# Optimization experiments

Measured on AMD Instinct MI355X. Metric: run time of the kernel, lower is better.

Reference implementation:

```python
import jax, jax.numpy as jnp
import numpy as np
from jax import lax

DIM = 64
HEADS = 4
GN_EPS = 1e-5
L2_EPS = 1e-12


def conv2d(x, w, b=None, pad=0, groups=1, dil=1):
    out = lax.conv_general_dilated(
        x, w, window_strides=(1, 1), padding=[(pad, pad), (pad, pad)],
        rhs_dilation=(dil, dil), dimension_numbers=('NCHW', 'OIHW', 'NCHW'),
        feature_group_count=groups)
    if b is not None:
        out = out + b[None, :, None, None]
    return out


def group_norm2(x, gamma, beta):
    # GroupNorm with 2 groups over (C/2, H, W)
    b, c, h, w = x.shape
    xr = x.reshape(b, 2, c // 2, h, w)
    mu = xr.mean(axis=(2, 3, 4), keepdims=True)
    var = xr.var(axis=(2, 3, 4), keepdims=True)
    xn = ((xr - mu) * lax.rsqrt(var + GN_EPS)).reshape(b, c, h, w)
    return xn * gamma[None, :, None, None] + beta[None, :, None, None]


def lka(x, c0w, c0b, csw, csb, c1w, c1b, gn_g, gn_b):
    dim = c0w.shape[0]
    a = conv2d(x, c0w, c0b, pad=2, groups=dim)           # depthwise 5x5
    a = conv2d(a, csw, csb, pad=3, groups=dim, dil=3)    # depthwise 3x3, dilation 3
    a = conv2d(a, c1w, c1b, pad=0)                       # 1x1 pointwise
    return jax.nn.leaky_relu(group_norm2(a, gn_g, gn_b), 0.2)


def l2norm_lastdim(t):
    n = jnp.sqrt(jnp.sum(t * t, axis=-1, keepdims=True))
    return t / jnp.maximum(n, L2_EPS)


def setup_inputs() -> dict:
    key = jax.random.key(0)
    ks = jax.random.split(key, 24)
    B, C, H, W = 4, DIM, 256, 256
    s = 0.05

    def rn(k, shape, scale=s):
        return jax.random.normal(k, shape, dtype=jnp.float32) * scale

    d2 = 2 * DIM
    inp = {
        'x': jax.random.normal(ks[0], (B, C, H, W), dtype=jnp.float32),
        'y': jax.random.normal(ks[1], (B, C, H, W), dtype=jnp.float32),
        # 1x1 projections (bias=False)
        'kv_w': rn(ks[2], (d2, DIM, 1, 1)),
        'q_w': rn(ks[3], (DIM, DIM, 1, 1)),
        'proj_w': rn(ks[4], (DIM, DIM, 1, 1)),
        # kv LKA (C_hid = C_out = 128)
        'kv_c0_w': rn(ks[5], (d2, 1, 5, 5)), 'kv_c0_b': rn(ks[6], (d2,)),
        'kv_cs_w': rn(ks[7], (d2, 1, 3, 3)), 'kv_cs_b': rn(ks[8], (d2,)),
        'kv_c1_w': rn(ks[9], (d2, d2, 1, 1)), 'kv_c1_b': rn(ks[10], (d2,)),
        'kv_gn_g': jnp.ones((d2,), jnp.float32), 'kv_gn_b': jnp.zeros((d2,), jnp.float32),
        # q LKA (C_hid = C_out = 64)
        'q_c0_w': rn(ks[11], (DIM, 1, 5, 5)), 'q_c0_b': rn(ks[12], (DIM,)),
        'q_cs_w': rn(ks[13], (DIM, 1, 3, 3)), 'q_cs_b': rn(ks[14], (DIM,)),
        'q_c1_w': rn(ks[15], (DIM, DIM, 1, 1)), 'q_c1_b': rn(ks[16], (DIM,)),
        'q_gn_g': jnp.ones((DIM,), jnp.float32), 'q_gn_b': jnp.zeros((DIM,), jnp.float32),
        'temperature': jnp.ones((HEADS, 1, 1), jnp.float32),
    }
    return inp


def reference(x, y, kv_w, q_w, proj_w,
              kv_c0_w, kv_c0_b, kv_cs_w, kv_cs_b, kv_c1_w, kv_c1_b, kv_gn_g, kv_gn_b,
              q_c0_w, q_c0_b, q_cs_w, q_cs_b, q_c1_w, q_c1_b, q_gn_g, q_gn_b,
              temperature):
    b, c, h, w = x.shape
    kv = lka(conv2d(y, kv_w), kv_c0_w, kv_c0_b, kv_cs_w, kv_cs_b, kv_c1_w, kv_c1_b, kv_gn_g, kv_gn_b)
    k, v = jnp.split(kv, 2, axis=1)
    q = lka(conv2d(x, q_w), q_c0_w, q_c0_b, q_cs_w, q_cs_b, q_c1_w, q_c1_b, q_gn_g, q_gn_b)

    ch = c // HEADS
    hw = h * w
    q = q.reshape(b, HEADS, ch, hw)
    k = k.reshape(b, HEADS, ch, hw)
    v = v.reshape(b, HEADS, ch, hw)

    q = l2norm_lastdim(q)
    k = l2norm_lastdim(k)

    attn = jnp.einsum('bhcn,bhdn->bhcd', q, k) * temperature[None]  # [b,H,ch,ch]
    attn = jax.nn.softmax(attn, axis=-1)
    out = jnp.einsum('bhcd,bhdn->bhcn', attn, v).reshape(b, c, h, w)
    return conv2d(out, proj_w)
```

## Files before the change

kernel.cpp:

```cpp
#include <hip/hip_runtime.h>

#define HW 65536
#define IMG 256

__device__ __forceinline__ float hsum4(float4 v) { return v.x + v.y + v.z + v.w; }
__device__ __forceinline__ float lrelu(float v) { return v >= 0.f ? v : 0.2f * v; }

template<int CIT, int NW, bool GNIN, bool DUAL>
__global__ __launch_bounds__(NW*64)
void conv1x1_v5(const float* __restrict__ in, int in_cs,
                const float* __restrict__ in2, int in2_cs,
                const float* __restrict__ w, int w_bstride,
                const float* __restrict__ bias,
                float* __restrict__ out, int out_cs, int out_coff,
                float* __restrict__ stats, int gsel,
                const float* __restrict__ gstats,
                const float* __restrict__ g_gamma, const float* __restrict__ g_beta,
                int g_coff, float g_Nf)
{
    const int b  = blockIdx.y;
    const int j  = threadIdx.x & 63;
    const int wv = __builtin_amdgcn_readfirstlane((int)(threadIdx.x >> 6));
    const int co0 = wv * 16;
    const int q0 = blockIdx.x * 64;
    const float* wb = w + (size_t)b * w_bstride;

    float gmean = 0.f, grstd = 0.f;
    if (GNIN) {
        gmean = gstats[b*4] / g_Nf;
        float var = gstats[b*4 + 1] / g_Nf - gmean * gmean;
        grstd = rsqrtf(var + 1e-5f);
    }

    float4 acc[16];
    #pragma unroll
    for (int k = 0; k < 16; ++k) {
        float bv = bias ? bias[co0 + k] : 0.f;
        acc[k] = make_float4(bv, bv, bv, bv);
    }

    const float4* in4a = (const float4*)in + (size_t)b * in_cs * (HW/4) + q0 + j;

    auto run = [&](const float4* base, const float* wrb, int n) {
        #pragma unroll 4
        for (int ci = 0; ci < n; ++ci) {
            float4 x = base[(size_t)ci * (HW/4)];
            if (GNIN) {
                float A = g_gamma[g_coff + ci] * grstd;
                float B = g_beta[g_coff + ci] - gmean * A;
                x.x = lrelu(fmaf(x.x, A, B));
                x.y = lrelu(fmaf(x.y, A, B));
                x.z = lrelu(fmaf(x.z, A, B));
                x.w = lrelu(fmaf(x.w, A, B));
            }
            const float* wr = wrb + ci;
            #pragma unroll
            for (int k = 0; k < 16; ++k) {
                float wk = wr[(size_t)(co0 + k) * CIT];
                acc[k].x = fmaf(wk, x.x, acc[k].x);
                acc[k].y = fmaf(wk, x.y, acc[k].y);
                acc[k].z = fmaf(wk, x.z, acc[k].z);
                acc[k].w = fmaf(wk, x.w, acc[k].w);
            }
        }
    };

    if (DUAL) {
        const float4* in4b = (const float4*)in2 + (size_t)b * in2_cs * (HW/4) + q0 + j;
        run(in4a, wb, 64);
        run(in4b, wb + 64, 64);
    } else {
        run(in4a, wb, CIT);
    }

    if (!GNIN && stats) {
        float s = 0.f, ss = 0.f;
        #pragma unroll
        for (int k = 0; k < 16; ++k) {
            s  += acc[k].x + acc[k].y + acc[k].z + acc[k].w;
            ss += acc[k].x*acc[k].x + acc[k].y*acc[k].y
                + acc[k].z*acc[k].z + acc[k].w*acc[k].w;
        }
        #pragma unroll
        for (int o = 32; o; o >>= 1) { s += __shfl_down(s, o, 64); ss += __shfl_down(ss, o, 64); }
        if (j == 0) {
            int g = 0;
            if (gsel == -1) g = (co0 >= 32) ? 1 : 0;
            else if (gsel == -2) g = (co0 >= 64) ? 1 : 0;
            float* st = stats + (size_t)b*4 + g*2;
            atomicAdd(st,     s);
            atomicAdd(st + 1, ss);
        }
    }

    float4* out4 = (float4*)out + ((size_t)b * out_cs + out_coff) * (HW/4) + q0 + j;
    #pragma unroll
    for (int k = 0; k < 16; ++k)
        out4[(size_t)(co0 + k) * (HW/4)] = acc[k];
}

__global__ __launch_bounds__(256)
void dwfused(const float* __restrict__ in, int in_cs, int in_coff,
             const float* __restrict__ w5, const float* __restrict__ b5, int w5_coff,
             const float* __restrict__ w3, const float* __restrict__ b3, int w3_coff,
             float* __restrict__ out, int out_cs, int out_coff)
{
    constexpr int TH = 32, TW = 64;
    constexpr int IN_H = TH + 10, IN_W = TW + 10;
    constexpr int MID_H = TH + 6, MID_W = TW + 6;
    constexpr int IN_RS = IN_W + 2;
    constexpr int MID_RS = MID_W + 2;
    __shared__ float Xs[IN_H * IN_RS];
    __shared__ float Ms[MID_H * MID_RS];
    const int z = blockIdx.z;
    const int c = z & 63, b = z >> 6;
    const int x0 = blockIdx.x * TW, y0 = blockIdx.y * TH;
    const float* ip = in + ((size_t)b*in_cs + in_coff + c) * HW;

    float wk5[25];
    #pragma unroll
    for (int i = 0; i < 25; ++i) wk5[i] = w5[(size_t)(w5_coff + c)*25 + i];
    const float bv5 = b5[w5_coff + c];
    float wk3[9];
    #pragma unroll
    for (int i = 0; i < 9; ++i) wk3[i] = w3[(size_t)(w3_coff + c)*9 + i];
    const float bv3 = b3[w3_coff + c];

    for (int idx = threadIdx.x; idx < IN_H*IN_W; idx += 256) {
        int ly = idx / IN_W, lx = idx - ly*IN_W;
        int gy = y0 + ly - 5, gx = x0 + lx - 5;
        float v = 0.f;
        if (gy >= 0 && gy < IMG && gx >= 0 && gx < IMG)
            v = ip[gy*IMG + gx];
        Xs[ly*IN_RS + lx] = v;
    }
    __syncthreads();

    for (int idx = threadIdx.x; idx < MID_H*MID_W; idx += 256) {
        int my = idx / MID_W, mx = idx - my*MID_W;
        int gy = y0 + my - 3, gx = x0 + mx - 3;
        float v = 0.f;
        if (gy >= 0 && gy < IMG && gx >= 0 && gx < IMG) {
            v = bv5;
            #pragma unroll
            for (int ky = 0; ky < 5; ++ky) {
                const float* xr = &Xs[(my + ky)*IN_RS + mx];
                #pragma unroll
                for (int kx = 0; kx < 5; ++kx)
                    v = fmaf(wk5[ky*5 + kx], xr[kx], v);
            }
        }
        Ms[my*MID_RS + mx] = v;
    }
    __syncthreads();

    const int qx = (threadIdx.x & 15) * 4;
    const int ly0 = threadIdx.x >> 4;
    float* op = out + ((size_t)b*out_cs + out_coff + c) * HW;
    #pragma unroll
    for (int r = 0; r < 2; ++r) {
        const int oy = ly0 + r*16;
        float o0 = bv3, o1 = bv3, o2 = bv3, o3 = bv3;
        #pragma unroll
        for (int kt = 0; kt < 3; ++kt) {
            const float* mr = &Ms[(oy + 3*kt)*MID_RS + qx];
            #pragma unroll
            for (int kx = 0; kx < 3; ++kx) {
                float wv_ = wk3[kt*3 + kx];
                o0 = fmaf(wv_, mr[3*kx + 0], o0);
                o1 = fmaf(wv_, mr[3*kx + 1], o1);
                o2 = fmaf(wv_, mr[3*kx + 2], o2);
                o3 = fmaf(wv_, mr[3*kx + 3], o3);
            }
        }
        *(float4*)(op + (size_t)(y0 + oy)*IMG + x0 + qx) = make_float4(o0, o1, o2, o3);
    }
}

__global__ __launch_bounds__(256)
void attn_dot_v4(const float* __restrict__ q, const float* __restrict__ k, int k_cs,
                 const float* __restrict__ stQ, const float* __restrict__ stK,
                 const float* __restrict__ qg, const float* __restrict__ qb,
                 const float* __restrict__ kg, const float* __restrict__ kb,
                 float* __restrict__ attn_raw,
                 float* __restrict__ ssq, float* __restrict__ ssk)
{
    __shared__ float4 qs[2048], ks[2048];
    __shared__ float sred[512];
    const int h = blockIdx.y, b = blockIdx.z;
    const int t0 = blockIdx.x * 128;
    const int cc = threadIdx.x & 15;
    const int ch = h*16 + cc;

    const int gq = (ch >= 32) ? 1 : 0;
    float mq = stQ[b*4 + gq*2] / (32.f * HW);
    float vq = stQ[b*4 + gq*2 + 1] / (32.f * HW) - mq*mq;
    const float Aq = qg[ch] * rsqrtf(vq + 1e-5f);
    const float Bq = qb[ch] - mq * Aq;
    float mk = stK[b*4] / (64.f * HW);
    float vk = stK[b*4 + 1] / (64.f * HW) - mk*mk;
    const float Ak = kg[ch] * rsqrtf(vk + 1e-5f);
    const float Bk = kb[ch] - mk * Ak;

    const float4* q4 = (const float4*)q + ((size_t)b*64   + ch) * (HW/4) + t0;
    const float4* k4 = (const float4*)k + ((size_t)b*k_cs + ch) * (HW/4) + t0;
    float sq_acc = 0.f, sk_acc = 0.f;
    #pragma unroll
    for (int s = 0; s < 8; ++s) {
        int t = (threadIdx.x >> 4) + s*16;
        float4 v = q4[t];
        v.x = lrelu(fmaf(v.x, Aq, Bq)); v.y = lrelu(fmaf(v.y, Aq, Bq));
        v.z = lrelu(fmaf(v.z, Aq, Bq)); v.w = lrelu(fmaf(v.w, Aq, Bq));
        sq_acc += v.x*v.x + v.y*v.y + v.z*v.z + v.w*v.w;
        qs[t*16 + cc] = v;
        float4 u = k4[t];
        u.x = lrelu(fmaf(u.x, Ak, Bk)); u.y = lrelu(fmaf(u.y, Ak, Bk));
        u.z = lrelu(fmaf(u.z, Ak, Bk)); u.w = lrelu(fmaf(u.w, Ak, Bk));
        sk_acc += u.x*u.x + u.y*u.y + u.z*u.z + u.w*u.w;
        ks[t*16 + cc] = u;
    }
    sred[threadIdx.x]       = sq_acc;
    sred[256 + threadIdx.x] = sk_acc;
    __syncthreads();

    const int p   = threadIdx.x & 63;
    const int sub = threadIdx.x >> 6;
    const int c0 = (p >> 3) << 1, d0 = (p & 7) << 1;
    float4 a00 = make_float4(0,0,0,0), a01 = a00, a10 = a00, a11 = a00;
    #pragma unroll
    for (int i = 0; i < 32; ++i) {
        int t = sub*32 + i;
        float4 qa = qs[t*16 + c0], qb_ = qs[t*16 + c0 + 1];
        float4 ka = ks[t*16 + d0], kb_ = ks[t*16 + d0 + 1];
        a00.x = fmaf(qa.x, ka.x, a00.x); a00.y = fmaf(qa.y, ka.y, a00.y);
        a00.z = fmaf(qa.z, ka.z, a00.z); a00.w = fmaf(qa.w, ka.w, a00.w);
        a01.x = fmaf(qa.x, kb_.x, a01.x); a01.y = fmaf(qa.y, kb_.y, a01.y);
        a01.z = fmaf(qa.z, kb_.z, a01.z); a01.w = fmaf(qa.w, kb_.w, a01.w);
        a10.x = fmaf(qb_.x, ka.x, a10.x); a10.y = fmaf(qb_.y, ka.y, a10.y);
        a10.z = fmaf(qb_.z, ka.z, a10.z); a10.w = fmaf(qb_.w, ka.w, a10.w);
        a11.x = fmaf(qb_.x, kb_.x, a11.x); a11.y = fmaf(qb_.y, kb_.y, a11.y);
        a11.z = fmaf(qb_.z, kb_.z, a11.z); a11.w = fmaf(qb_.w, kb_.w, a11.w);
    }
    float* ar = attn_raw + ((size_t)b*4 + h) * 256;
    atomicAdd(&ar[(c0  )*16 + d0  ], hsum4(a00));
    atomicAdd(&ar[(c0  )*16 + d0+1], hsum4(a01));
    atomicAdd(&ar[(c0+1)*16 + d0  ], hsum4(a10));
    atomicAdd(&ar[(c0+1)*16 + d0+1], hsum4(a11));

    if (threadIdx.x < 16) {
        float s = 0.f;
        #pragma unroll
        for (int jj = 0; jj < 16; ++jj) s += sred[threadIdx.x + 16*jj];
        atomicAdd(&ssq[b*64 + h*16 + threadIdx.x], s);
    } else if (threadIdx.x < 32) {
        const int c2 = threadIdx.x - 16;
        float s = 0.f;
        #pragma unroll
        for (int jj = 0; jj < 16; ++jj) s += sred[256 + c2 + 16*jj];
        atomicAdd(&ssk[b*64 + h*16 + c2], s);
    }
}

__global__ __launch_bounds__(256)
void attn_softmax_v2(const float* __restrict__ attn_raw,
                     const float* __restrict__ ssq, const float* __restrict__ ssk,
                     const float* __restrict__ temp, float* __restrict__ attn)
{
    const int h = blockIdx.x, b = blockIdx.y;
    const int c = threadIdx.x >> 4, d = threadIdx.x & 15;
    const float nq = fmaxf(sqrtf(ssq[b*64 + h*16 + c]), 1e-12f);
    const float nk = fmaxf(sqrtf(ssk[b*64 + h*16 + d]), 1e-12f);
    float logit = attn_raw[((size_t)b*4 + h)*256 + c*16 + d] / (nq * nk) * temp[h];
    float m = logit;
    #pragma unroll
    for (int o = 8; o; o >>= 1) m = fmaxf(m, __shfl_xor(m, o, 16));
    float e = expf(logit - m);
    float s = e;
    #pragma unroll
    for (int o = 8; o; o >>= 1) s += __shfl_xor(s, o, 16);
    attn[((size_t)b*4 + h)*256 + c*16 + d] = e / s;
}

__global__ __launch_bounds__(256)
void build_m_v2(const float* __restrict__ attn, const float* __restrict__ proj_w,
                float* __restrict__ M)
{
    const int b = blockIdx.x;
    for (int i = threadIdx.x; i < 4096; i += 256) {
        int co = i >> 6, ci = i & 63;
        int h = ci >> 4, d = ci & 15;
        float s = 0.f;
        #pragma unroll
        for (int cc = 0; cc < 16; ++cc)
            s += proj_w[co*64 + h*16 + cc] * attn[((size_t)b*4 + h)*256 + cc*16 + d];
        M[(size_t)b*4096 + i] = s;
    }
}

extern "C" void kernel_launch(void* const* d_in, const int* in_sizes, int n_in,
                              void* d_out, int out_size, void* d_ws, size_t ws_size,
                              hipStream_t stream)
{
    const float* x       = (const float*)d_in[0];
    const float* y       = (const float*)d_in[1];
    const float* kv_w    = (const float*)d_in[2];
    const float* q_w     = (const float*)d_in[3];
    const float* proj_w  = (const float*)d_in[4];
    const float* kv_c0_w = (const float*)d_in[5];
    const float* kv_c0_b = (const float*)d_in[6];
    const float* kv_cs_w = (const float*)d_in[7];
    const float* kv_cs_b = (const float*)d_in[8];
    const float* kv_c1_w = (const float*)d_in[9];
    const float* kv_c1_b = (const float*)d_in[10];
    const float* kv_gn_g = (const float*)d_in[11];
    const float* kv_gn_b = (const float*)d_in[12];
    const float* q_c0_w  = (const float*)d_in[13];
    const float* q_c0_b  = (const float*)d_in[14];
    const float* q_cs_w  = (const float*)d_in[15];
    const float* q_cs_b  = (const float*)d_in[16];
    const float* q_c1_w  = (const float*)d_in[17];
    const float* q_c1_b  = (const float*)d_in[18];
    const float* q_gn_g  = (const float*)d_in[19];
    const float* q_gn_b  = (const float*)d_in[20];
    const float* temp    = (const float*)d_in[21];

    float* ws       = (float*)d_ws;
    float* statsKV  = ws;
    float* statsQ   = ws + 16;
    float* sumsq_k  = ws + 32;
    float* sumsq_q  = ws + 288;
    float* attn_raw = ws + 544;
    float* attn     = ws + 4640;
    float* Mw       = ws + 8736;
    float* big      = (float*)((char*)d_ws + 131072);

    const size_t perb_bytes = (size_t)192 * HW * 4;
    int nb = 1;
    if      (ws_size >= 131072 + 4*perb_bytes) nb = 4;
    else if (ws_size >= 131072 + 2*perb_bytes) nb = 2;

    hipMemsetAsync(d_ws, 0, 102400, stream);
    dim3 blk(256);

    for (int b0 = 0; b0 < 4; b0 += nb) {
        const float* xb = x + (size_t)b0*64*HW;
        const float* yb = y + (size_t)b0*64*HW;
        float* H1 = big;
        float* H2 = big + (size_t)nb*128*HW;
        float* O  = (float*)d_out + (size_t)b0*64*HW;
        float* stK = statsKV + b0*4;
        float* stQ = statsQ  + b0*4;
        float* ssk = sumsq_k + b0*64;
        float* ssq = sumsq_q + b0*64;
        float* arw = attn_raw + b0*1024;
        float* atn = attn     + b0*1024;
        float* Mb  = Mw       + b0*4096;

        dim3 gdwf(4, 8, nb*64);
        dim3 gc(256, nb);

        conv1x1_v5<64,8,false,false><<<gc, dim3(512), 0, stream>>>(
            yb, 64, nullptr, 0, kv_w, 0, nullptr, H1, 128, 0,
            nullptr, 0, nullptr, nullptr, nullptr, 0, 0.f);
        dwfused<<<gdwf, blk, 0, stream>>>(H1, 128, 0,  kv_c0_w, kv_c0_b, 0,  kv_cs_w, kv_cs_b, 0,  H2, 64, 0);
        dwfused<<<gdwf, blk, 0, stream>>>(H1, 128, 64, kv_c0_w, kv_c0_b, 64, kv_cs_w, kv_cs_b, 64, O,  64, 0);
        conv1x1_v5<128,8,false,true><<<gc, dim3(512), 0, stream>>>(
            H2, 64, O, 64, kv_c1_w, 0, kv_c1_b, H1, 128, 0,
            stK, -2, nullptr, nullptr, nullptr, 0, 0.f);

        conv1x1_v5<64,4,false,false><<<gc, blk, 0, stream>>>(
            xb, 64, nullptr, 0, q_w, 0, nullptr, O, 64, 0,
            nullptr, 0, nullptr, nullptr, nullptr, 0, 0.f);
        dwfused<<<gdwf, blk, 0, stream>>>(O, 64, 0, q_c0_w, q_c0_b, 0, q_cs_w, q_cs_b, 0, H2, 64, 0);
        conv1x1_v5<64,4,false,false><<<gc, blk, 0, stream>>>(
            H2, 64, nullptr, 0, q_c1_w, 0, q_c1_b, O, 64, 0,
            stQ, -1, nullptr, nullptr, nullptr, 0, 0.f);

        attn_dot_v4<<<dim3(128,4,nb), blk, 0, stream>>>(O, H1, 128, stQ, stK,
                                                        q_gn_g, q_gn_b, kv_gn_g, kv_gn_b,
                                                        arw, ssq, ssk);
        attn_softmax_v2<<<dim3(4,nb), blk, 0, stream>>>(arw, ssq, ssk, temp, atn);
        build_m_v2<<<dim3(nb), blk, 0, stream>>>(atn, proj_w, Mb);

        conv1x1_v5<64,4,true,false><<<gc, blk, 0, stream>>>(
            H1 + (size_t)64*HW, 128, nullptr, 0, Mw + b0*4096, 4096, nullptr,
            (float*)d_out + (size_t)b0*64*HW, 64, 0,
            nullptr, 0, stK+2, kv_gn_g, kv_gn_b, 64, 64.f*HW);
    }
}
```

Baseline: 1.040 ms.

## Stage 1x1-conv input channels through double-buffered LDS via async global-to-LDS loads

The pointwise conv kernel previously had every wave read all input channels from global memory on its own. Now each block stages 8 input channels at a time into a double-buffered LDS tile using global_load_lds, one channel per wave. All waves then read the shared tile, and the next chunk's load is issued before computing the current one. The 64-output-channel variants also move to 512 threads with 8 output channels per wave, which lowers accumulator register pressure. The cost is an LDS round trip plus a block barrier per chunk, and correctness depends on the async LDS loads having completed by each barrier.

```diff
diff --git a/kernel.cpp b/kernel.cpp
--- a/kernel.cpp
+++ b/kernel.cpp
@@ -6,9 +6,15 @@
 __device__ __forceinline__ float hsum4(float4 v) { return v.x + v.y + v.z + v.w; }
 __device__ __forceinline__ float lrelu(float v) { return v >= 0.f ? v : 0.2f * v; }
 
-template<int CIT, int NW, bool GNIN, bool DUAL>
-__global__ __launch_bounds__(NW*64)
-void conv1x1_v5(const float* __restrict__ in, int in_cs,
+typedef const __attribute__((address_space(1))) unsigned int guint;
+typedef __attribute__((address_space(3))) unsigned int luint;
+__device__ __forceinline__ void gload_lds16(const float4* g, float4* l) {
+    __builtin_amdgcn_global_load_lds((guint*)(const void*)g, (luint*)(void*)l, 16, 0, 0);
+}
+
+template<int CIT, int CO, bool GNIN, bool DUAL>
+__global__ __launch_bounds__(512)
+void conv1x1_v6(const float* __restrict__ in, int in_cs,
                 const float* __restrict__ in2, int in2_cs,
                 const float* __restrict__ w, int w_bstride,
                 const float* __restrict__ bias,
@@ -18,11 +24,17 @@
                 const float* __restrict__ g_gamma, const float* __restrict__ g_beta,
                 int g_coff, float g_Nf)
 {
+    constexpr int COPW = CO / 8;
+    constexpr int NCHUNK = CIT / 8;
+    __shared__ float4 Xs[2][8 * 64];
     const int b  = blockIdx.y;
     const int j  = threadIdx.x & 63;
     const int wv = __builtin_amdgcn_readfirstlane((int)(threadIdx.x >> 6));
-    const int co0 = wv * 16;
+    const int co0 = wv * COPW;
     const int q0 = blockIdx.x * 64;
+    const float4* in4a = (const float4*)in + (size_t)b * in_cs * (HW/4) + q0 + j;
+    const float4* in4b = DUAL ? ((const float4*)in2 + (size_t)b * in2_cs * (HW/4) + q0 + j)
+                              : nullptr;
     const float* wb = w + (size_t)b * w_bstride;
 
     float gmean = 0.f, grstd = 0.f;
@@ -32,30 +44,37 @@
         grstd = rsqrtf(var + 1e-5f);
     }
 
-    float4 acc[16];
-    #pragma unroll
-    for (int k = 0; k < 16; ++k) {
+    float4 acc[COPW];
+    #pragma unroll
+    for (int k = 0; k < COPW; ++k) {
         float bv = bias ? bias[co0 + k] : 0.f;
         acc[k] = make_float4(bv, bv, bv, bv);
     }
 
-    const float4* in4a = (const float4*)in + (size_t)b * in_cs * (HW/4) + q0 + j;
-
-    auto run = [&](const float4* base, const float* wrb, int n) {
-        #pragma unroll 4
-        for (int ci = 0; ci < n; ++ci) {
-            float4 x = base[(size_t)ci * (HW/4)];
+    auto stage = [&](int ch, int bsel) {
+        const int gci = ch * 8 + wv;
+        const float4* src = (DUAL && gci >= 64)
+            ? in4b + (size_t)(gci - 64) * (HW/4)
+            : in4a + (size_t)gci * (HW/4);
+        gload_lds16(src, &Xs[bsel][wv * 64]);
+    };
+
+    auto compute = [&](int ch, int bsel) {
+        #pragma unroll
+        for (int cl = 0; cl < 8; ++cl) {
+            const int gci = ch * 8 + cl;
+            float4 x = Xs[bsel][cl * 64 + j];
             if (GNIN) {
-                float A = g_gamma[g_coff + ci] * grstd;
-                float B = g_beta[g_coff + ci] - gmean * A;
+                float A = g_gamma[g_coff + gci] * grstd;
+                float B = g_beta[g_coff + gci] - gmean * A;
                 x.x = lrelu(fmaf(x.x, A, B));
                 x.y = lrelu(fmaf(x.y, A, B));
                 x.z = lrelu(fmaf(x.z, A, B));
                 x.w = lrelu(fmaf(x.w, A, B));
             }
-            const float* wr = wrb + ci;
+            const float* wr = wb + gci;
             #pragma unroll
-            for (int k = 0; k < 16; ++k) {
+            for (int k = 0; k < COPW; ++k) {
                 float wk = wr[(size_t)(co0 + k) * CIT];
                 acc[k].x = fmaf(wk, x.x, acc[k].x);
                 acc[k].y = fmaf(wk, x.y, acc[k].y);
@@ -65,18 +84,19 @@
         }
     };
 
-    if (DUAL) {
-        const float4* in4b = (const float4*)in2 + (size_t)b * in2_cs * (HW/4) + q0 + j;
-        run(in4a, wb, 64);
-        run(in4b, wb + 64, 64);
-    } else {
-        run(in4a, wb, CIT);
+    stage(0, 0);
+    __syncthreads();
+    #pragma unroll
+    for (int ch = 0; ch < NCHUNK; ++ch) {
+        if (ch + 1 < NCHUNK) stage(ch + 1, (ch + 1) & 1);
+        compute(ch, ch & 1);
+        __syncthreads();
     }
 
     if (!GNIN && stats) {
         float s = 0.f, ss = 0.f;
         #pragma unroll
-        for (int k = 0; k < 16; ++k) {
+        for (int k = 0; k < COPW; ++k) {
             s  += acc[k].x + acc[k].y + acc[k].z + acc[k].w;
             ss += acc[k].x*acc[k].x + acc[k].y*acc[k].y
                 + acc[k].z*acc[k].z + acc[k].w*acc[k].w;
@@ -95,7 +115,7 @@
 
     float4* out4 = (float4*)out + ((size_t)b * out_cs + out_coff) * (HW/4) + q0 + j;
     #pragma unroll
-    for (int k = 0; k < 16; ++k)
+    for (int k = 0; k < COPW; ++k)
         out4[(size_t)(co0 + k) * (HW/4)] = acc[k];
 }
 
@@ -341,6 +361,7 @@
 
     hipMemsetAsync(d_ws, 0, 102400, stream);
     dim3 blk(256);
+    dim3 blk5(512);
 
     for (int b0 = 0; b0 < 4; b0 += nb) {
         const float* xb = x + (size_t)b0*64*HW;
@@ -359,20 +380,20 @@
         dim3 gdwf(4, 8, nb*64);
         dim3 gc(256, nb);
 
-        conv1x1_v5<64,8,false,false><<<gc, dim3(512), 0, stream>>>(
+        conv1x1_v6<64,128,false,false><<<gc, blk5, 0, stream>>>(
             yb, 64, nullptr, 0, kv_w, 0, nullptr, H1, 128, 0,
             nullptr, 0, nullptr, nullptr, nullptr, 0, 0.f);
         dwfused<<<gdwf, blk, 0, stream>>>(H1, 128, 0,  kv_c0_w, kv_c0_b, 0,  kv_cs_w, kv_cs_b, 0,  H2, 64, 0);
         dwfused<<<gdwf, blk, 0, stream>>>(H1, 128, 64, kv_c0_w, kv_c0_b, 64, kv_cs_w, kv_cs_b, 64, O,  64, 0);
-        conv1x1_v5<128,8,false,true><<<gc, dim3(512), 0, stream>>>(
+        conv1x1_v6<128,128,false,true><<<gc, blk5, 0, stream>>>(
             H2, 64, O, 64, kv_c1_w, 0, kv_c1_b, H1, 128, 0,
             stK, -2, nullptr, nullptr, nullptr, 0, 0.f);
 
-        conv1x1_v5<64,4,false,false><<<gc, blk, 0, stream>>>(
+        conv1x1_v6<64,64,false,false><<<gc, blk5, 0, stream>>>(
             xb, 64, nullptr, 0, q_w, 0, nullptr, O, 64, 0,
             nullptr, 0, nullptr, nullptr, nullptr, 0, 0.f);
         dwfused<<<gdwf, blk, 0, stream>>>(O, 64, 0, q_c0_w, q_c0_b, 0, q_cs_w, q_cs_b, 0, H2, 64, 0);
-        conv1x1_v5<64,4,false,false><<<gc, blk, 0, stream>>>(
+        conv1x1_v6<64,64,false,false><<<gc, blk5, 0, stream>>>(
             H2, 64, nullptr, 0, q_c1_w, 0, q_c1_b, O, 64, 0,
             stQ, -1, nullptr, nullptr, nullptr, 0, 0.f);
 
@@ -382,7 +403,7 @@
         attn_softmax_v2<<<dim3(4,nb), blk, 0, stream>>>(arw, ssq, ssk, temp, atn);
         build_m_v2<<<dim3(nb), blk, 0, stream>>>(atn, proj_w, Mb);
 
-        conv1x1_v5<64,4,true,false><<<gc, blk, 0, stream>>>(
+        conv1x1_v6<64,64,true,false><<<gc, blk5, 0, stream>>>(
             H1 + (size_t)64*HW, 128, nullptr, 0, Mw + b0*4096, 4096, nullptr,
             (float*)d_out + (size_t)b0*64*HW, 64, 0,
             nullptr, 0, stK+2, kv_gn_g, kv_gn_b, 64, 64.f*HW);
```

New measurement: 1.604 ms. +54.3%, slower.

## Store intermediates in tiled pixel-block layout and widen conv1x1 tiles

Applied to the files above, without the earlier changes.

Intermediate activations move from plain NCHW planes to a blocked layout where each 512-pixel tile (two image rows) holds all channels contiguously. The 1x1 conv, depthwise and attention kernels are rewritten to read and write this layout. The 1x1 conv now uses 128-pixel by full-output-channel blocks of 512 or 1024 threads. The aim is more contiguous memory streams for the channel reductions and more reuse of each input read across output channels. The cost is larger blocks with lower occupancy, and the depthwise halo loads now stride across tiles.

```diff
diff --git a/kernel.cpp b/kernel.cpp
--- a/kernel.cpp
+++ b/kernel.cpp
@@ -6,9 +6,9 @@
 __device__ __forceinline__ float hsum4(float4 v) { return v.x + v.y + v.z + v.w; }
 __device__ __forceinline__ float lrelu(float v) { return v >= 0.f ? v : 0.2f * v; }
 
-template<int CIT, int NW, bool GNIN, bool DUAL>
-__global__ __launch_bounds__(NW*64)
-void conv1x1_v5(const float* __restrict__ in, int in_cs,
+template<int CIT, int CO, bool GNIN, bool DUAL, bool INB, bool OUTB>
+__global__ __launch_bounds__(CO*8)
+void conv1x1_v7(const float* __restrict__ in, int in_cs, int in_coff,
                 const float* __restrict__ in2, int in2_cs,
                 const float* __restrict__ w, int w_bstride,
                 const float* __restrict__ bias,
@@ -19,10 +19,10 @@
                 int g_coff, float g_Nf)
 {
     const int b  = blockIdx.y;
-    const int j  = threadIdx.x & 63;
-    const int wv = __builtin_amdgcn_readfirstlane((int)(threadIdx.x >> 6));
-    const int co0 = wv * 16;
-    const int q0 = blockIdx.x * 64;
+    const int T  = blockIdx.x;
+    const int q  = threadIdx.x & 127;
+    const int coh = __builtin_amdgcn_readfirstlane((int)(threadIdx.x >> 7));
+    const int co0 = coh * 16;
     const float* wb = w + (size_t)b * w_bstride;
 
     float gmean = 0.f, grstd = 0.f;
@@ -39,21 +39,23 @@
         acc[k] = make_float4(bv, bv, bv, bv);
     }
 
-    const float4* in4a = (const float4*)in + (size_t)b * in_cs * (HW/4) + q0 + j;
-
-    auto run = [&](const float4* base, const float* wrb, int n) {
+    auto run = [&](const float4* t4, int cs, int coff, const float* wrb, int gci0, int n) {
+        const float4* base = INB
+            ? t4 + ((size_t)T * cs + coff) * 128 + q
+            : t4 + (size_t)coff * (HW/4) + (size_t)T * 128 + q;
+        const size_t cstr = INB ? 128 : (HW/4);
         #pragma unroll 4
         for (int ci = 0; ci < n; ++ci) {
-            float4 x = base[(size_t)ci * (HW/4)];
+            float4 x = base[(size_t)ci * cstr];
             if (GNIN) {
-                float A = g_gamma[g_coff + ci] * grstd;
-                float B = g_beta[g_coff + ci] - gmean * A;
+                float A = g_gamma[g_coff + gci0 + ci] * grstd;
+                float B = g_beta[g_coff + gci0 + ci] - gmean * A;
                 x.x = lrelu(fmaf(x.x, A, B));
                 x.y = lrelu(fmaf(x.y, A, B));
                 x.z = lrelu(fmaf(x.z, A, B));
                 x.w = lrelu(fmaf(x.w, A, B));
             }
-            const float* wr = wrb + ci;
+            const float* wr = wrb + gci0 + ci;
             #pragma unroll
             for (int k = 0; k < 16; ++k) {
                 float wk = wr[(size_t)(co0 + k) * CIT];
@@ -65,12 +67,13 @@
         }
     };
 
+    const float4* inA = (const float4*)in + (size_t)b * in_cs * (HW/4);
     if (DUAL) {
-        const float4* in4b = (const float4*)in2 + (size_t)b * in2_cs * (HW/4) + q0 + j;
-        run(in4a, wb, 64);
-        run(in4b, wb + 64, 64);
+        const float4* inB = (const float4*)in2 + (size_t)b * in2_cs * (HW/4);
+        run(inA, in_cs, in_coff, wb, 0, 64);
+        run(inB, in2_cs, 0, wb, 64, 64);
     } else {
-        run(in4a, wb, CIT);
+        run(inA, in_cs, in_coff, wb, 0, CIT);
     }
 
     if (!GNIN && stats) {
@@ -83,7 +86,7 @@
         }
         #pragma unroll
         for (int o = 32; o; o >>= 1) { s += __shfl_down(s, o, 64); ss += __shfl_down(ss, o, 64); }
-        if (j == 0) {
+        if ((threadIdx.x & 63) == 0) {
             int g = 0;
             if (gsel == -1) g = (co0 >= 32) ? 1 : 0;
             else if (gsel == -2) g = (co0 >= 64) ? 1 : 0;
@@ -93,10 +96,14 @@
         }
     }
 
-    float4* out4 = (float4*)out + ((size_t)b * out_cs + out_coff) * (HW/4) + q0 + j;
-    #pragma unroll
-    for (int k = 0; k < 16; ++k)
-        out4[(size_t)(co0 + k) * (HW/4)] = acc[k];
+    float4* ob = (float4*)out + (size_t)b * out_cs * (HW/4);
+    #pragma unroll
+    for (int k = 0; k < 16; ++k) {
+        if (OUTB)
+            ob[((size_t)T * out_cs + out_coff + co0 + k) * 128 + q] = acc[k];
+        else
+            ob[(size_t)(out_coff + co0 + k) * (HW/4) + (size_t)T * 128 + q] = acc[k];
+    }
 }
 
 __global__ __launch_bounds__(256)
@@ -115,7 +122,7 @@
     const int z = blockIdx.z;
     const int c = z & 63, b = z >> 6;
     const int x0 = blockIdx.x * TW, y0 = blockIdx.y * TH;
-    const float* ip = in + ((size_t)b*in_cs + in_coff + c) * HW;
+    const float* ib = in + (size_t)b * in_cs * HW;
 
     float wk5[25];
     #pragma unroll
@@ -131,7 +138,7 @@
         int gy = y0 + ly - 5, gx = x0 + lx - 5;
         float v = 0.f;
         if (gy >= 0 && gy < IMG && gx >= 0 && gx < IMG)
-            v = ip[gy*IMG + gx];
+            v = ib[((size_t)(gy >> 1) * in_cs + in_coff + c) * 512 + (gy & 1) * 256 + gx];
         Xs[ly*IN_RS + lx] = v;
     }
     __syncthreads();
@@ -156,7 +163,7 @@
 
     const int qx = (threadIdx.x & 15) * 4;
     const int ly0 = threadIdx.x >> 4;
-    float* op = out + ((size_t)b*out_cs + out_coff + c) * HW;
+    float* ob = out + (size_t)b * out_cs * HW;
     #pragma unroll
     for (int r = 0; r < 2; ++r) {
         const int oy = ly0 + r*16;
@@ -173,12 +180,15 @@
                 o3 = fmaf(wv_, mr[3*kx + 3], o3);
             }
         }
-        *(float4*)(op + (size_t)(y0 + oy)*IMG + x0 + qx) = make_float4(o0, o1, o2, o3);
+        const int y = y0 + oy;
+        *(float4*)(ob + ((size_t)(y >> 1) * out_cs + out_coff + c) * 512 + (y & 1) * 256 + x0 + qx) =
+            make_float4(o0, o1, o2, o3);
     }
 }
 
 __global__ __launch_bounds__(256)
-void attn_dot_v4(const float* __restrict__ q, const float* __restrict__ k, int k_cs,
+void attn_dot_v5(const float* __restrict__ qt, int q_cs,
+                 const float* __restrict__ kt, int k_cs,
                  const float* __restrict__ stQ, const float* __restrict__ stK,
                  const float* __restrict__ qg, const float* __restrict__ qb,
                  const float* __restrict__ kg, const float* __restrict__ kb,
@@ -188,7 +198,7 @@
     __shared__ float4 qs[2048], ks[2048];
     __shared__ float sred[512];
     const int h = blockIdx.y, b = blockIdx.z;
-    const int t0 = blockIdx.x * 128;
+    const int T = blockIdx.x;
     const int cc = threadIdx.x & 15;
     const int ch = h*16 + cc;
 
@@ -202,8 +212,8 @@
     const float Ak = kg[ch] * rsqrtf(vk + 1e-5f);
     const float Bk = kb[ch] - mk * Ak;
 
-    const float4* q4 = (const float4*)q + ((size_t)b*64   + ch) * (HW/4) + t0;
-    const float4* k4 = (const float4*)k + ((size_t)b*k_cs + ch) * (HW/4) + t0;
+    const float4* q4 = (const float4*)qt + (size_t)b*q_cs*(HW/4) + ((size_t)T*q_cs + ch)*128;
+    const float4* k4 = (const float4*)kt + (size_t)b*k_cs*(HW/4) + ((size_t)T*k_cs + ch)*128;
     float sq_acc = 0.f, sk_acc = 0.f;
     #pragma unroll
     for (int s = 0; s < 8; ++s) {
@@ -357,33 +367,33 @@
         float* Mb  = Mw       + b0*4096;
 
         dim3 gdwf(4, 8, nb*64);
-        dim3 gc(256, nb);
-
-        conv1x1_v5<64,8,false,false><<<gc, dim3(512), 0, stream>>>(
-            yb, 64, nullptr, 0, kv_w, 0, nullptr, H1, 128, 0,
+        dim3 gcv(128, nb);
+
+        conv1x1_v7<64,128,false,false,false,true><<<gcv, dim3(1024), 0, stream>>>(
+            yb, 64, 0, nullptr, 0, kv_w, 0, nullptr, H1, 128, 0,
             nullptr, 0, nullptr, nullptr, nullptr, 0, 0.f);
         dwfused<<<gdwf, blk, 0, stream>>>(H1, 128, 0,  kv_c0_w, kv_c0_b, 0,  kv_cs_w, kv_cs_b, 0,  H2, 64, 0);
         dwfused<<<gdwf, blk, 0, stream>>>(H1, 128, 64, kv_c0_w, kv_c0_b, 64, kv_cs_w, kv_cs_b, 64, O,  64, 0);
-        conv1x1_v5<128,8,false,true><<<gc, dim3(512), 0, stream>>>(
-            H2, 64, O, 64, kv_c1_w, 0, kv_c1_b, H1, 128, 0,
+        conv1x1_v7<128,128,false,true,true,true><<<gcv, dim3(1024), 0, stream>>>(
+            H2, 64, 0, O, 64, kv_c1_w, 0, kv_c1_b, H1, 128, 0,
             stK, -2, nullptr, nullptr, nullptr, 0, 0.f);
 
-        conv1x1_v5<64,4,false,false><<<gc, blk, 0, stream>>>(
-            xb, 64, nullptr, 0, q_w, 0, nullptr, O, 64, 0,
+        conv1x1_v7<64,64,false,false,false,true><<<gcv, dim3(512), 0, stream>>>(
+            xb, 64, 0, nullptr, 0, q_w, 0, nullptr, O, 64, 0,
             nullptr, 0, nullptr, nullptr, nullptr, 0, 0.f);
         dwfused<<<gdwf, blk, 0, stream>>>(O, 64, 0, q_c0_w, q_c0_b, 0, q_cs_w, q_cs_b, 0, H2, 64, 0);
-        conv1x1_v5<64,4,false,false><<<gc, blk, 0, stream>>>(
-            H2, 64, nullptr, 0, q_c1_w, 0, q_c1_b, O, 64, 0,
+        conv1x1_v7<64,64,false,false,true,true><<<gcv, dim3(512), 0, stream>>>(
+            H2, 64, 0, nullptr, 0, q_c1_w, 0, q_c1_b, O, 64, 0,
             stQ, -1, nullptr, nullptr, nullptr, 0, 0.f);
 
-        attn_dot_v4<<<dim3(128,4,nb), blk, 0, stream>>>(O, H1, 128, stQ, stK,
+        attn_dot_v5<<<dim3(128,4,nb), blk, 0, stream>>>(O, 64, H1, 128, stQ, stK,
                                                         q_gn_g, q_gn_b, kv_gn_g, kv_gn_b,
                                                         arw, ssq, ssk);
         attn_softmax_v2<<<dim3(4,nb), blk, 0, stream>>>(arw, ssq, ssk, temp, atn);
         build_m_v2<<<dim3(nb), blk, 0, stream>>>(atn, proj_w, Mb);
 
-        conv1x1_v5<64,4,true,false><<<gc, blk, 0, stream>>>(
-            H1 + (size_t)64*HW, 128, nullptr, 0, Mw + b0*4096, 4096, nullptr,
+        conv1x1_v7<64,64,true,false,true,false><<<gcv, dim3(512), 0, stream>>>(
+            H1, 128, 64, nullptr, 0, Mw + b0*4096, 4096, nullptr,
             (float*)d_out + (size_t)b0*64*HW, 64, 0,
             nullptr, 0, stK+2, kv_gn_g, kv_gn_b, 64, 64.f*HW);
     }
```

After: 1.017 ms. -2.1%, faster.
